# Performance work log

Measured on AMD Instinct MI355X. Metric: run time of the kernel, lower is better.

Reference implementation:

```python
import jax, jax.numpy as jnp
import numpy as np
from jax import lax

H = 12  # num_heads (from init_kwargs)


def _orthogonal_landmarks(q, num_landmarks):
    # q: (B, N, D) already scaled. Faithful to torch loop: recursively pick the
    # point whose max |cos sim| to the already-selected landmarks is minimal.
    B, N, D = q.shape
    nrm = jnp.linalg.norm(q, axis=-1, keepdims=True)
    qk = q / jnp.maximum(nrm, 1e-12)
    bidx = jnp.arange(B)
    key = jax.random.key(42)
    idx0 = jax.random.randint(key, (B,), 0, N)
    cur = qk[bidx, idx0]                             # (B, D)
    # running max |cos sim|; selected rows pinned to 10 (as in torch code)
    max_sim = jnp.zeros((B, N), qk.dtype).at[bidx, idx0].set(10.0)

    def step(carry, _):
        max_sim, cur = carry
        cos = jnp.abs(jnp.einsum('bnd,bd->bn', qk, cur))
        max_sim = jnp.maximum(max_sim, cos)
        idx = jnp.argmin(max_sim, axis=-1)
        cur2 = qk[bidx, idx]
        max_sim = max_sim.at[bidx, idx].set(10.0)
        return (max_sim, cur2), idx

    (_, _), idxs = lax.scan(step, (max_sim, cur), None, length=num_landmarks - 1)
    all_idx = jnp.concatenate([idx0[None, :], idxs], axis=0).T  # (B, L)
    landmarks = q[bidx[:, None], all_idx]                        # unnormalized q rows
    return lax.stop_gradient(landmarks)


def _orthoformer(q, k, v, num_landmarks, num_frames):
    # q,k,v: (B*h, N, D);  N = F * P
    Bh, N, D = q.shape
    F = num_frames
    P = N // F
    sc = D ** (-0.25)
    q = q * sc
    k = k * sc
    lm = _orthogonal_landmarks(q, num_landmarks)                 # (Bh, L, D)
    kernel_1 = jax.nn.softmax(jnp.einsum('bnd,bld->bnl', q, lm), axis=-1)   # (Bh,N,L)
    k2 = jnp.einsum('bld,bnd->bln', lm, k).reshape(Bh, num_landmarks, F, P)
    kernel_2 = jax.nn.softmax(k2, axis=-1)                       # (Bh,L,F,P)
    vr = v.reshape(Bh, F, P, D)
    x = jnp.einsum('blfp,bfpd->blfd', kernel_2, vr)
    x = jnp.einsum('bnl,blfd->bnfd', kernel_1, x)                # (Bh,N,F,D)
    return x


def setup_inputs() -> dict:
    key = jax.random.key(0)
    ks = jax.random.split(key, 6)
    B, F, P, C = 2, 16, 196, 768
    N = F * P
    s = 0.02
    x = jax.random.normal(ks[0], (B, N, C), jnp.float32)
    W_qkv = jax.random.normal(ks[1], (C, 3 * C), jnp.float32) * s
    W_pq = jax.random.normal(ks[2], (C, C), jnp.float32) * s
    W_pkv = jax.random.normal(ks[3], (C, 2 * C), jnp.float32) * s
    W_proj = jax.random.normal(ks[4], (C, C), jnp.float32) * s
    b_proj = jnp.zeros((C,), jnp.float32)
    return {"x": x, "W_qkv": W_qkv, "W_pq": W_pq, "W_pkv": W_pkv,
            "W_proj": W_proj, "b_proj": b_proj,
            "seq_len": P, "num_frames": F, "num_landmarks": 128}


def reference(x, W_qkv, W_pq, W_pkv, W_proj, b_proj, seq_len, num_frames, num_landmarks):
    B, N, C = x.shape
    F, P, h = num_frames, seq_len, H
    d = C // h
    scale = d ** (-0.5)
    qkv = x @ W_qkv                                              # (B,N,3C)
    q, k, v = jnp.split(qkv, 3, axis=-1)
    def to_bh(t):  # b n (h d) -> (b h) n d
        return t.reshape(B, N, h, d).transpose(0, 2, 1, 3).reshape(B * h, N, d)
    q_, k_, v_ = to_bh(q), to_bh(k), to_bh(v)
    xo = _orthoformer(q_, k_, v_, num_landmarks, F)              # (B*h,N,F,d)
    # (b h) s f d -> b s f (h d)
    xo = xo.reshape(B, h, N, F, d).transpose(0, 2, 3, 1, 4).reshape(B, N, F, C)
    # diagonal over (frame-of-query g, frame-of-key f)
    xd = xo.reshape(B, F, P, F, C)
    xdiag = jnp.diagonal(xd, axis1=1, axis2=3)                   # (B,P,C,F)
    xdiag = jnp.moveaxis(xdiag, -1, 1).reshape(B, N, C)          # b (f p) d
    q2 = xdiag @ W_pq                                            # (B,N,C)
    k2, v2 = jnp.split(xo @ W_pkv, 2, axis=-1)                   # (B,N,F,C) each
    q2 = q2.reshape(B, N, h, d).transpose(0, 2, 1, 3) * scale    # (B,h,N,d)
    k2 = k2.reshape(B, N, F, h, d).transpose(0, 3, 1, 2, 4)      # (B,h,N,F,d)
    v2 = v2.reshape(B, N, F, h, d).transpose(0, 3, 1, 2, 4)
    attn = jax.nn.softmax(jnp.einsum('bhsd,bhsfd->bhsf', q2, k2), axis=-1)
    out = jnp.einsum('bhsf,bhsfd->bhsd', attn, v2)               # (B,h,N,d)
    out = out.transpose(0, 2, 1, 3).reshape(B, N, C)
    out = out @ W_proj + b_proj
    return out, attn
```

## Files before the change

kernel.cpp:

```cpp
#include <hip/hip_runtime.h>


using u16 = unsigned short;
using u32 = unsigned int;
using u64 = unsigned long long;

typedef short bf16x8 __attribute__((ext_vector_type(8)));
typedef float f32x4 __attribute__((ext_vector_type(4)));

#define N_ 3136
#define C_ 768
#define H_ 12
#define F_ 16
#define P_ 196
#define L_ 128
#define SC_ 0.35355339059327373f
#define OUTPART_ ((size_t)2 * N_ * C_)
#define KB_ 8
#define RPB_ 392

__device__ __forceinline__ float b2f(u16 u) {
  u32 x = ((u32)u) << 16; float f; __builtin_memcpy(&f, &x, 4); return f;
}
__device__ __forceinline__ float lo16f(u32 u) {
  u32 x = u << 16; float f; __builtin_memcpy(&f, &x, 4); return f;
}
__device__ __forceinline__ float hi16f(u32 u) {
  u32 x = u & 0xFFFF0000u; float f; __builtin_memcpy(&f, &x, 4); return f;
}
__device__ __forceinline__ u16 f2b(float f) {
  u32 u; __builtin_memcpy(&u, &f, 4);
  u32 r = (u + 0x7FFFu + ((u >> 16) & 1u)) >> 16;
  return (u16)r;
}
__device__ __forceinline__ u64 d2u(double d) { u64 u; __builtin_memcpy(&u, &d, 8); return u; }

__device__ __forceinline__ void gll16(const void* g, void* l) {
  __builtin_amdgcn_global_load_lds(
      (__attribute__((address_space(1))) void*)g,
      (__attribute__((address_space(3))) void*)l, 16, 0, 0);
}

__global__ void detect_k(const u32* __restrict__ w, int* __restrict__ flag) {
  const int t = threadIdx.x;
  int hits = 0;
  #pragma unroll
  for (int i = 0; i < 16; ++i) {
    u32 word = w[t * 16 + i];
    u32 e = (word >> 7) & 0xFFu;
    if (e >= 110u && e <= 126u) hits++;
  }
  #pragma unroll
  for (int off = 32; off > 0; off >>= 1) hits += __shfl_down(hits, off);
  if (t == 0) flag[0] = (hits >= 512) ? 0 : 1;
}

__global__ void zcnt_k(u64* __restrict__ p) { if (threadIdx.x < 384) p[threadIdx.x] = 0ull; }

__device__ __forceinline__ void tf2(u32 k0, u32 k1v, u32 c0, u32 c1, u32& o0, u32& o1) {
  u32 ks[3] = {k0, k1v, k0 ^ k1v ^ 0x1BD11BDAu};
  u32 x0 = c0 + ks[0], x1 = c1 + ks[1];
  const u32 rA[4] = {13u, 15u, 26u, 6u}, rB[4] = {17u, 29u, 16u, 24u};
  #pragma unroll
  for (int r = 0; r < 5; ++r) {
    #pragma unroll
    for (int q = 0; q < 4; ++q) {
      u32 rot = (r & 1) ? rB[q] : rA[q];
      x0 += x1; x1 = (x1 << rot) | (x1 >> (32u - rot)); x1 ^= x0;
    }
    x0 += ks[(r + 1) % 3];
    x1 += ks[(r + 2) % 3] + (u32)(r + 1);
  }
  o0 = x0; o1 = x1;
}

__device__ __forceinline__ int tf_idx0(int bh) {
  u32 a0, a1, b0, b1;
  tf2(0u, 42u, 0u, 0u, a0, a1);
  tf2(0u, 42u, 0u, 1u, b0, b1);
  u32 j = (u32)bh;
  u32 h0, h1, l0, l1;
  tf2(a0, a1, 0u, j, h0, h1);
  u32 hi = h0 ^ h1;
  tf2(b0, b1, 0u, j, l0, l1);
  u32 lo = l0 ^ l1;
  return (int)(((hi % 3136u) * 2048u + (lo % 3136u)) % 3136u);
}

__global__ __launch_bounds__(256) void qselT_k(const void* __restrict__ xr, const void* __restrict__ wr,
                                               const int* __restrict__ flagp, float* __restrict__ qt)
{
  __shared__ float As[128 * 20];
  __shared__ float Bs[16 * 64];
  const int t = threadIdx.x;
  const int m0 = blockIdx.x * 128;
  const int n0 = blockIdx.y * 64;
  const int f32i = flagp[0];
  const int tx = t & 15, ty = t >> 4;
  float acc[8][4];
  #pragma unroll
  for (int i = 0; i < 8; ++i)
    #pragma unroll
    for (int j = 0; j < 4; ++j) acc[i][j] = 0.f;

  const int alr = t >> 1;
  const int alk = (t & 1) * 8;
  const int bkr = t >> 4;
  const int bnc = (t & 15) * 4;

  for (int k0 = 0; k0 < 768; k0 += 16) {
    float av[8];
    float4 bv;
    if (f32i) {
      const float* xa = (const float*)xr + (size_t)(m0 + alr) * 768 + k0 + alk;
      float4 a0 = *(const float4*)(xa);
      float4 a1 = *(const float4*)(xa + 4);
      av[0] = a0.x; av[1] = a0.y; av[2] = a0.z; av[3] = a0.w;
      av[4] = a1.x; av[5] = a1.y; av[6] = a1.z; av[7] = a1.w;
      bv = *(const float4*)((const float*)wr + (size_t)(k0 + bkr) * 2304 + n0 + bnc);
    } else {
      const u16* xa = (const u16*)xr + (size_t)(m0 + alr) * 768 + k0 + alk;
      #pragma unroll
      for (int j = 0; j < 8; ++j) av[j] = b2f(xa[j]);
      const u16* wa = (const u16*)wr + (size_t)(k0 + bkr) * 2304 + n0 + bnc;
      bv.x = b2f(wa[0]); bv.y = b2f(wa[1]); bv.z = b2f(wa[2]); bv.w = b2f(wa[3]);
    }
    #pragma unroll
    for (int j = 0; j < 8; ++j) As[alr * 20 + alk + j] = av[j];
    *(float4*)(&Bs[bkr * 64 + bnc]) = bv;
    __syncthreads();
    #pragma unroll
    for (int kk = 0; kk < 16; ++kk) {
      float a[8], b[4];
      #pragma unroll
      for (int i = 0; i < 8; ++i) a[i] = As[(ty * 8 + i) * 20 + kk];
      #pragma unroll
      for (int j = 0; j < 4; ++j) b[j] = Bs[kk * 64 + tx * 4 + j];
      #pragma unroll
      for (int i = 0; i < 8; ++i)
        #pragma unroll
        for (int j = 0; j < 4; ++j) acc[i][j] += a[i] * b[j];
    }
    __syncthreads();
  }
  #pragma unroll
  for (int i = 0; i < 8; ++i) {
    const int m = m0 + ty * 8 + i;
    const int b = m / N_, n = m - b * N_;
    #pragma unroll
    for (int j = 0; j < 4; ++j) {
      const int col = n0 + tx * 4 + j;
      const int hh = col >> 6, dd = col & 63;
      qt[((size_t)(b * H_ + hh) * 64 + dd) * N_ + n] = acc[i][j] * SC_;
    }
  }
}

__global__ __launch_bounds__(512, 1) void landmarksR_k(
    const float* __restrict__ qt, float* __restrict__ lm, u64* __restrict__ cand)
{
  const int kb = blockIdx.y;
  const int bh = blockIdx.x;
  const float* QT = qt + (size_t)bh * 64 * N_;
  float* LM = lm + (size_t)bh * L_ * 64;
  u64* cd = cand + (size_t)bh * 16;
  __shared__ double curD[64];
  __shared__ u64 redV[8];
  __shared__ int redI[8];
  __shared__ int sW;
  const int t = threadIdx.x;
  const bool act = (t < RPB_);
  const int g = t >> 2, dc = t & 3, d0 = dc * 16;
  const int r0 = kb * RPB_;
  const int myRow = r0 + t;
  const float* base = QT + r0 + 4 * g;

  float4 qreg[16];
  #pragma unroll
  for (int i = 0; i < 16; ++i) qreg[i] = (float4){0.f, 0.f, 0.f, 0.f};
  if (act) {
    #pragma unroll
    for (int i = 0; i < 16; ++i) qreg[i] = *(const float4*)(base + (size_t)(d0 + i) * N_);
  }

  double inv_own = 0.0, ms_own = 0.0;
  if (act) {
    double s0 = 0.0, s1 = 0.0, s2 = 0.0, s3 = 0.0;
    #pragma unroll
    for (int i = 0; i < 16; ++i) {
      const float4 v = qreg[i];
      s0 += (double)v.x * (double)v.x; s1 += (double)v.y * (double)v.y;
      s2 += (double)v.z * (double)v.z; s3 += (double)v.w * (double)v.w;
    }
    s0 += __shfl_xor(s0, 1); s1 += __shfl_xor(s1, 1);
    s2 += __shfl_xor(s2, 1); s3 += __shfl_xor(s3, 1);
    s0 += __shfl_xor(s0, 2); s1 += __shfl_xor(s1, 2);
    s0 = s0; s1 = s1;
    s2 += __shfl_xor(s2, 2); s3 += __shfl_xor(s3, 2);
    const double sown = (dc == 0) ? s0 : (dc == 1) ? s1 : (dc == 2) ? s2 : s3;
    inv_own = 1.0 / fmax(sqrt(sown), 1e-12);
  }
  const int idx0 = tf_idx0(bh);
  if (act && myRow == idx0) ms_own = 10.0;

  if (t < 64) {
    const float vf = QT[(size_t)t * N_ + idx0];
    double v = (double)vf;
    double s = v * v;
    #pragma unroll
    for (int off = 32; off; off >>= 1) s += __shfl_xor(s, off);
    curD[t] = v / fmax(sqrt(s), 1e-12);
    if (kb == 0) LM[t] = vf;
  }
  __syncthreads();

  for (int step = 1; step < 128; ++step) {
    u64 bV = d2u(1e30); int bI = 0x7fffffff;
    if (act) {
      double a0 = 0.0, a1 = 0.0, a2 = 0.0, a3 = 0.0;
      #pragma unroll
      for (int i = 0; i < 16; ++i) {
        const float4 v = qreg[i];
        const double c = curD[d0 + i];
        a0 += (double)v.x * c; a1 += (double)v.y * c;
        a2 += (double)v.z * c; a3 += (double)v.w * c;
      }
      a0 += __shfl_xor(a0, 1); a1 += __shfl_xor(a1, 1);
      a2 += __shfl_xor(a2, 1); a3 += __shfl_xor(a3, 1);
      a0 += __shfl_xor(a0, 2); a1 += __shfl_xor(a1, 2);
      a2 += __shfl_xor(a2, 2); a3 += __shfl_xor(a3, 2);
      const double aown = (dc == 0) ? a0 : (dc == 1) ? a1 : (dc == 2) ? a2 : a3;
      ms_own = fmax(ms_own, fabs(aown * inv_own));
      bV = d2u(ms_own); bI = myRow;
    }
    #pragma unroll
    for (int off = 32; off; off >>= 1) {
      const u64 ov = __shfl_xor(bV, off);
      const int oi = __shfl_xor(bI, off);
      if (ov < bV || (ov == bV && oi < bI)) { bV = ov; bI = oi; }
    }
    if ((t & 63) == 0) { redV[t >> 6] = bV; redI[t >> 6] = bI; }
    __syncthreads();
    const int par = step & 1;
    if (t == 0) {
      u64 v = redV[0]; int ix = redI[0];
      #pragma unroll
      for (int w2 = 1; w2 < 8; ++w2)
        if (redV[w2] < v || (redV[w2] == v && redI[w2] < ix)) { v = redV[w2]; ix = redI[w2]; }
      const u64 pk = (v & ~((1ull << 19) - 1ull)) | ((u64)(u32)(step & 127) << 12) | (u64)(u32)ix;
      __hip_atomic_store(&cd[par * KB_ + kb], pk, __ATOMIC_RELAXED, __HIP_MEMORY_SCOPE_AGENT);
    }
    if (t < 64) {
      u64 pv = ~0ull;
      int ok = 1;
      for (;;) {
        if (t < KB_) {
          pv = __hip_atomic_load(&cd[par * KB_ + t], __ATOMIC_RELAXED, __HIP_MEMORY_SCOPE_AGENT);
          ok = ((int)((pv >> 12) & 127u) == step) ? 1 : 0;
        }
        if (__all(ok)) break;
        __builtin_amdgcn_s_sleep(1);
      }
      u64 m = (t < KB_) ? pv : ~0ull;
      #pragma unroll
      for (int off = 1; off < KB_; off <<= 1) {
        const u64 o = __shfl_xor(m, off);
        if (o < m) m = o;
      }
      if (t == 0) sW = (int)(m & 0xFFFu);
    }
    __syncthreads();
    const int w = sW;
    if (act && myRow == w) ms_own = 10.0;
    if (t < 64) {
      const float vf = QT[(size_t)t * N_ + w];
      double v = (double)vf;
      double s = v * v;
      #pragma unroll
      for (int off = 32; off; off >>= 1) s += __shfl_xor(s, off);
      curD[t] = v / fmax(sqrt(s), 1e-12);
      if (kb == 0) LM[(size_t)step * 64 + t] = vf;
    }
    __syncthreads();
  }
}

__device__ __forceinline__ void twT_body(const void* W, int K, int Nn, int f32i,
                                         u16* WT, int k0, int n0, int t, u16 (&Ts)[64][80])
{
  const int kr = t >> 2, nc = (t & 3) * 16;
  u16 tmp[16];
  if (f32i) {
    const float* p = (const float*)W + (size_t)(k0 + kr) * Nn + n0 + nc;
    #pragma unroll
    for (int j = 0; j < 16; ++j) tmp[j] = f2b(p[j]);
  } else {
    const u16* p = (const u16*)W + (size_t)(k0 + kr) * Nn + n0 + nc;
    #pragma unroll
    for (int j = 0; j < 16; ++j) tmp[j] = p[j];
  }
  #pragma unroll
  for (int j = 0; j < 16; ++j) Ts[kr][nc + j] = tmp[j];
  __syncthreads();
  const int nr = t >> 2, kc = (t & 3) * 16;
  u16 o[16];
  #pragma unroll
  for (int j = 0; j < 16; ++j) o[j] = Ts[kc + j][nr];
  u16* dst = WT + (size_t)(n0 + nr) * K + k0 + kc;
  *(uint4*)(dst) = *(uint4*)(o);
  *(uint4*)(dst + 8) = *(uint4*)(o + 8);
}

__global__ __launch_bounds__(256) void twT_k(const void* __restrict__ W, int K, int Nn,
                                             const int* __restrict__ flagp, u16* __restrict__ WT)
{
  __shared__ u16 Ts[64][80];
  twT_body(W, K, Nn, flagp[0], WT, blockIdx.x * 64, blockIdx.y * 64, threadIdx.x, Ts);
}

__global__ __launch_bounds__(256) void twT3_k(const void* __restrict__ W0, const void* __restrict__ W1,
                                              const void* __restrict__ W2, const int* __restrict__ flagp,
                                              u16* __restrict__ T0, u16* __restrict__ T1, u16* __restrict__ T2,
                                              u16* __restrict__ Wb)
{
  __shared__ u16 Ts[64][80];
  const int z = blockIdx.z;
  const int t = threadIdx.x;
  if (z == 3) {
    const int k0 = blockIdx.x * 64, n0 = blockIdx.y * 64;
    const int kr = t >> 2, nc = (t & 3) * 16;
    u16 tmp[16];
    if (flagp[0]) {
      const float* p = (const float*)W0 + (size_t)(k0 + kr) * 1536 + n0 + nc;
      #pragma unroll
      for (int j = 0; j < 16; ++j) tmp[j] = f2b(p[j]);
    } else {
      const u16* p = (const u16*)W0 + (size_t)(k0 + kr) * 1536 + n0 + nc;
      #pragma unroll
      for (int j = 0; j < 16; ++j) tmp[j] = p[j];
    }
    u16* dst = Wb + (size_t)(k0 + kr) * 1536 + n0 + nc;
    *(uint4*)(dst) = *(uint4*)(tmp);
    *(uint4*)(dst + 8) = *(uint4*)(tmp + 8);
    return;
  }
  const void* W = (z == 0) ? W0 : (z == 1) ? W1 : W2;
  u16* WT = (z == 0) ? T0 : (z == 1) ? T1 : T2;
  const int Nn = (z == 0) ? 1536 : 768;
  if (blockIdx.y * 64 >= Nn) return;
  twT_body(W, 768, Nn, flagp[0], WT, blockIdx.x * 64, blockIdx.y * 64, t, Ts);
}

__global__ __launch_bounds__(256) void xcvt_k(const void* __restrict__ x,
                                              const int* __restrict__ flagp, u16* __restrict__ xb)
{
  const int i = blockIdx.x * 256 + threadIdx.x;
  if (flagp[0]) {
    const float4* p = (const float4*)x + (size_t)i * 2;
    float4 f0 = p[0], f1 = p[1];
    u16 tmp[8] = { f2b(f0.x), f2b(f0.y), f2b(f0.z), f2b(f0.w),
                   f2b(f1.x), f2b(f1.y), f2b(f1.z), f2b(f1.w) };
    *(uint4*)(xb + (size_t)i * 8) = *(uint4*)tmp;
  } else {
    ((uint4*)xb)[i] = ((const uint4*)x)[i];
  }
}

struct GemmCore {
  const u16 *aP0, *aP1, *bP0, *bP1;
  u16 *lA0, *lA1, *lB0, *lB1;
  int roA[4], roB[4];
  int mw, nw, lr, lk;
};

__device__ __forceinline__ void gemm_core_init(GemmCore& gc, u16* As, u16* Bs,
    const u16* A16, const u16* B16, size_t aOff, size_t bOff,
    int m0, int n0, int lda, int ldb, int M, int t)
{
  const int lane = t & 63;
  const int w = t >> 6;
  gc.mw = (w >> 1) * 64;
  gc.nw = (w & 1) * 64;
  gc.lr = lane & 15;
  gc.lk = lane >> 4;
  const int c0 = w * 2, c1 = c0 + 1;
  const int rl = lane >> 2, sl = lane & 3;
  const int rowA0 = c0 * 16 + rl, rowA1 = c1 * 16 + rl;
  const int segA0 = (sl ^ ((rowA0 ^ (rowA0 >> 2)) & 3)) * 8;
  const int segA1 = (sl ^ ((rowA1 ^ (rowA1 >> 2)) & 3)) * 8;
  int ga0 = m0 + rowA0; if (ga0 >= M) ga0 = M - 1;
  int ga1 = m0 + rowA1; if (ga1 >= M) ga1 = M - 1;
  gc.aP0 = A16 + aOff + (size_t)ga0 * lda + segA0;
  gc.aP1 = A16 + aOff + (size_t)ga1 * lda + segA1;
  gc.bP0 = B16 + bOff + (size_t)(n0 + rowA0) * ldb + segA0;
  gc.bP1 = B16 + bOff + (size_t)(n0 + rowA1) * ldb + segA1;
  gc.lA0 = &As[c0 * 512]; gc.lA1 = &As[c1 * 512];
  gc.lB0 = &Bs[c0 * 512]; gc.lB1 = &Bs[c1 * 512];
  #pragma unroll
  for (int q = 0; q < 4; ++q) {
    const int ra = gc.mw + q * 16 + gc.lr;
    gc.roA[q] = ra * 32 + ((gc.lk ^ ((ra ^ (ra >> 2)) & 3)) * 8);
    const int rb = gc.nw + q * 16 + gc.lr;
    gc.roB[q] = rb * 32 + ((gc.lk ^ ((rb ^ (rb >> 2)) & 3)) * 8);
  }
}

__device__ __forceinline__ void gemm_core_loop(const GemmCore& gc, u16* As, u16* Bs,
                                               int K, f32x4 (&acc)[4][4])
{
  for (int k0 = 0; k0 < K; k0 += 32) {
    gll16(gc.aP0 + k0, gc.lA0);
    gll16(gc.aP1 + k0, gc.lA1);
    gll16(gc.bP0 + k0, gc.lB0);
    gll16(gc.bP1 + k0, gc.lB1);
    __syncthreads();
    bf16x8 af[4], bfv[4];
    #pragma unroll
    for (int mt = 0; mt < 4; ++mt) af[mt] = *(const bf16x8*)(&As[gc.roA[mt]]);
    #pragma unroll
    for (int nt = 0; nt < 4; ++nt) bfv[nt] = *(const bf16x8*)(&Bs[gc.roB[nt]]);
    #pragma unroll
    for (int mt = 0; mt < 4; ++mt)
      #pragma unroll
      for (int nt = 0; nt < 4; ++nt)
        acc[mt][nt] = __builtin_amdgcn_mfma_f32_16x16x32_bf16(af[mt], bfv[nt], acc[mt][nt], 0, 0, 0);
    __syncthreads();
  }
}

template <int MODE>
__global__ __launch_bounds__(256) void gemm_k(
    const void* __restrict__ Ap, const void* __restrict__ Bp,
    int M, int K, int lda, int ldb, int n0c, int cn, const int* __restrict__ flagp,
    float* __restrict__ of0, u16* __restrict__ ob0, u16* __restrict__ ob1, u16* __restrict__ ob2,
    const void* __restrict__ biasRaw, void* __restrict__ outRaw)
{
  __shared__ u16 As[128 * 32];
  __shared__ u16 Bs[128 * 32];
  const int t = threadIdx.x;
  const int m0 = blockIdx.x * 128;
  const int n0 = blockIdx.y * 128;
  const int rf = (MODE == 4) ? flagp[0] : 0;

  size_t aOff = 0, bOff = 0;
  if constexpr (MODE == 1) {
    const int bh = blockIdx.z;
    aOff = (size_t)bh * ((size_t)N_ * 128) + (size_t)n0c * 128;
    bOff = (size_t)bh * (1024 * 128);
  }
  if constexpr (MODE == 5) {
    const int h = blockIdx.z;
    aOff = (size_t)h * (2 * cn) * 64;
    bOff = (size_t)h * 64;
  }
  if constexpr (MODE == 6) {
    const int h = blockIdx.z;
    aOff = (size_t)h * (2 * cn) * 768;
    bOff = (size_t)(768 + h * 64) * 768;
  }
  f32x4 acc[4][4];
  #pragma unroll
  for (int i = 0; i < 4; ++i)
    #pragma unroll
    for (int j = 0; j < 4; ++j) acc[i][j] = (f32x4){0.f, 0.f, 0.f, 0.f};

  GemmCore gc;
  gemm_core_init(gc, As, Bs, (const u16*)Ap, (const u16*)Bp, aOff, bOff, m0, n0, lda, ldb, M, t);
  gemm_core_loop(gc, As, Bs, K, acc);

  const int lr = gc.lr, lk = gc.lk, mw = gc.mw, nw = gc.nw;
  #pragma unroll
  for (int mt = 0; mt < 4; ++mt) {
    #pragma unroll
    for (int nt = 0; nt < 4; ++nt) {
      #pragma unroll
      for (int r = 0; r < 4; ++r) {
        const int grow = m0 + mw + mt * 16 + lk * 4 + r;
        const int gcol = n0 + nw + nt * 16 + lr;
        if (grow >= M) continue;
        float vv = acc[mt][nt][r];
        if constexpr (MODE == 0) {
          int b = (grow >= N_) ? 1 : 0;
          int n = grow - b * N_;
          int t3 = gcol / C_, cc = gcol - t3 * C_;
          int hh = cc >> 6, dd = cc & 63;
          size_t dst = (((size_t)(b * H_ + hh)) * N_ + n) * 64 + dd;
          if (t3 == 0) ob0[dst] = f2b(vv * SC_);
          else if (t3 == 1) ob1[dst] = f2b(vv * SC_);
          else ob2[dst] = f2b(vv);
        } else if constexpr (MODE == 1) {
          const int bh = blockIdx.z;
          int b = bh / H_, hh = bh - b * H_;
          int f = gcol >> 6, dd = gcol & 63;
          u16 wv = f2b(vv);
          ob0[(((size_t)(b * cn + grow)) * F_ + f) * C_ + hh * 64 + dd] = wv;
          int n = n0c + grow;
          if (f == n / P_) ob1[((size_t)(b * cn + grow)) * C_ + hh * 64 + dd] = wv;
        } else if constexpr (MODE == 3) {
          int hh = gcol >> 6, dd = gcol & 63;
          ob0[((size_t)hh * (2 * cn) + grow) * 64 + dd] = f2b(vv * 0.125f);
        } else if constexpr (MODE == 5) {
          ob0[((size_t)blockIdx.z * (2 * cn) + grow) * 768 + gcol] = f2b(vv);
        } else if constexpr (MODE == 6) {
          if (gcol < 64) {
            int b2 = (grow >= cn) ? 1 : 0;
            int ln = grow - b2 * cn;
            ob0[((size_t)(b2 * N_ + n0c + ln)) * 768 + blockIdx.z * 64 + gcol] = f2b(vv);
          }
        } else {
          float bvad = rf ? ((const float*)biasRaw)[gcol] : b2f(((const u16*)biasRaw)[gcol]);
          float ov = vv + bvad;
          if (rf) ((float*)outRaw)[(size_t)grow * C_ + gcol] = ov;
          else    ((u16*)outRaw)[(size_t)grow * C_ + gcol] = f2b(ov);
        }
      }
    }
  }
}

__global__ __launch_bounds__(256) void k1_k(const u16* __restrict__ qb,
                                            const float* __restrict__ lm,
                                            u16* __restrict__ k1)
{
  const int bh = blockIdx.y;
  const int r0 = blockIdx.x * 64;
  __shared__ float qT[64][65];
  __shared__ float lmS[128 * 64];
  __shared__ float redA[4][64];
  __shared__ float redB[64];
  const int t = threadIdx.x;
  const u16* Q = qb + ((size_t)bh * N_ + r0) * 64;
  const float* Lm = lm + (size_t)bh * L_ * 64;
  for (int u = t; u < 2048; u += 256) ((float4*)lmS)[u] = ((const float4*)Lm)[u];
  for (int u = t; u < 512; u += 256) {
    int row = u >> 3, j0 = (u & 7) * 8;
    uint4 pk = *(const uint4*)(Q + (size_t)row * 64 + j0);
    const u16* pu = (const u16*)&pk;
    #pragma unroll
    for (int jj = 0; jj < 8; ++jj) qT[j0 + jj][row] = b2f(pu[jj]);
  }
  __syncthreads();
  const int row = t & 63, ch = t >> 6;
  float qr[64];
  #pragma unroll
  for (int j = 0; j < 64; ++j) qr[j] = qT[j][row];
  float s[32];
  for (int li = 0; li < 32; ++li) {
    const float* lp = lmS + (ch * 32 + li) * 64;
    float a = 0.f;
    #pragma unroll
    for (int j = 0; j < 64; ++j) a += lp[j] * qr[j];
    s[li] = a;
  }
  float mx = -1e30f;
  for (int li = 0; li < 32; ++li) mx = fmaxf(mx, s[li]);
  redA[ch][row] = mx;
  __syncthreads();
  if (t < 64) redB[t] = fmaxf(fmaxf(redA[0][t], redA[1][t]), fmaxf(redA[2][t], redA[3][t]));
  __syncthreads();
  mx = redB[row];
  float sum = 0.f;
  for (int li = 0; li < 32; ++li) { float e = __expf(s[li] - mx); s[li] = e; sum += e; }
  __syncthreads();
  redA[ch][row] = sum;
  __syncthreads();
  if (t < 64) redB[t] = 1.0f / (redA[0][t] + redA[1][t] + redA[2][t] + redA[3][t]);
  __syncthreads();
  const float inv = redB[row];
  u16* out = k1 + ((size_t)bh * N_ + r0 + row) * 128 + ch * 32;
  for (int li = 0; li < 32; ++li) out[li] = f2b(s[li] * inv);
}

__global__ __launch_bounds__(256) void k2x1_k(const float* __restrict__ lm,
                                              const u16* __restrict__ kb,
                                              const u16* __restrict__ vb,
                                              u16* __restrict__ x1)
{
  const int bh = blockIdx.x;
  const int f = blockIdx.y;
  __shared__ u16 kS[P_ * 64];
  __shared__ u16 vS[P_ * 64];
  __shared__ float redM[2][128];
  __shared__ float redS[2][128];
  const int t = threadIdx.x;
  const u16* Kf = kb + ((size_t)bh * N_ + f * P_) * 64;
  const u16* Vf = vb + ((size_t)bh * N_ + f * P_) * 64;
  for (int u = t; u < 1568; u += 256) {
    ((uint4*)kS)[u] = ((const uint4*)Kf)[u];
    ((uint4*)vS)[u] = ((const uint4*)Vf)[u];
  }
  __syncthreads();
  const int l = t & 127, half = t >> 7;
  const float* lp = lm + ((size_t)bh * L_ + l) * 64;
  float lr[64];
  #pragma unroll
  for (int j = 0; j < 64; ++j) lr[j] = lp[j];

  const int p0 = half * 98, p1 = p0 + 98;
  float mx = -1e30f;
  for (int p = p0; p < p1; ++p) {
    const uint4* kp = (const uint4*)(kS + p * 64);
    float s = 0.f;
    #pragma unroll
    for (int q4 = 0; q4 < 8; ++q4) {
      uint4 pk = kp[q4];
      const u32* pu = (const u32*)&pk;
      #pragma unroll
      for (int j2 = 0; j2 < 4; ++j2) {
        u32 u = pu[j2];
        s += lr[q4 * 8 + j2 * 2] * lo16f(u) + lr[q4 * 8 + j2 * 2 + 1] * hi16f(u);
      }
    }
    mx = fmaxf(mx, s);
  }
  redM[half][l] = mx;
  __syncthreads();
  mx = fmaxf(redM[0][l], redM[1][l]);

  float sm = 0.f;
  for (int p = p0; p < p1; ++p) {
    const uint4* kp = (const uint4*)(kS + p * 64);
    float s = 0.f;
    #pragma unroll
    for (int q4 = 0; q4 < 8; ++q4) {
      uint4 pk = kp[q4];
      const u32* pu = (const u32*)&pk;
      #pragma unroll
      for (int j2 = 0; j2 < 4; ++j2) {
        u32 u = pu[j2];
        s += lr[q4 * 8 + j2 * 2] * lo16f(u) + lr[q4 * 8 + j2 * 2 + 1] * hi16f(u);
      }
    }
    sm += __expf(s - mx);
  }
  redS[half][l] = sm;
  __syncthreads();
  const float inv = 1.0f / (redS[0][l] + redS[1][l]);

  const int dd0 = half * 32;
  float acc[32];
  #pragma unroll
  for (int u = 0; u < 32; ++u) acc[u] = 0.f;
  for (int p = 0; p < P_; ++p) {
    const uint4* kp = (const uint4*)(kS + p * 64);
    float s = 0.f;
    #pragma unroll
    for (int q4 = 0; q4 < 8; ++q4) {
      uint4 pk = kp[q4];
      const u32* pu = (const u32*)&pk;
      #pragma unroll
      for (int j2 = 0; j2 < 4; ++j2) {
        u32 u = pu[j2];
        s += lr[q4 * 8 + j2 * 2] * lo16f(u) + lr[q4 * 8 + j2 * 2 + 1] * hi16f(u);
      }
    }
    const float e = __expf(s - mx);
    const uint4* vp = (const uint4*)(vS + p * 64 + dd0);
    #pragma unroll
    for (int q4 = 0; q4 < 4; ++q4) {
      uint4 pv = vp[q4];
      const u32* pu = (const u32*)&pv;
      #pragma unroll
      for (int j2 = 0; j2 < 4; ++j2) {
        u32 u = pu[j2];
        acc[q4 * 8 + j2 * 2]     += e * lo16f(u);
        acc[q4 * 8 + j2 * 2 + 1] += e * hi16f(u);
      }
    }
  }
  u16* outT = x1 + (size_t)bh * (1024 * 128) + (size_t)(f * 64 + dd0) * 128 + l;
  for (int u = 0; u < 32; ++u) outT[(size_t)u * 128] = f2b(acc[u] * inv);
}

__global__ __launch_bounds__(256) void attn2_k(const u16* __restrict__ xoc,
                                               const u16* __restrict__ g,
                                               int n0c, int cn, const int* __restrict__ flagp,
                                               void* __restrict__ outRaw, u16* __restrict__ wc)
{
  __shared__ float aS[12][16];
  const int t = threadIdx.x;
  const int m = blockIdx.x;
  const int b = (m >= cn) ? 1 : 0;
  const int ln = m - b * cn;
  const int n = n0c + ln;
  const int f32o = flagp[0];
  const u16* Xo = xoc + ((size_t)(b * cn + ln) * 16) * 768;
  const size_t hstr = (size_t)(2 * cn) * 768;

  if (t < 192) {
    const int h = t >> 4, f = t & 15;
    const uint4* xp = (const uint4*)(Xo + (size_t)f * 768);
    const uint4* gp = (const uint4*)(g + (size_t)h * hstr + (size_t)m * 768);
    float lg = 0.f;
    #pragma unroll 4
    for (int q = 0; q < 96; ++q) {
      uint4 xv = xp[q], gv = gp[q];
      const u32* xu = (const u32*)&xv;
      const u32* gu = (const u32*)&gv;
      #pragma unroll
      for (int j = 0; j < 4; ++j)
        lg += lo16f(xu[j]) * lo16f(gu[j]) + hi16f(xu[j]) * hi16f(gu[j]);
    }
    float mx = lg;
    mx = fmaxf(mx, __shfl_xor(mx, 1));
    mx = fmaxf(mx, __shfl_xor(mx, 2));
    mx = fmaxf(mx, __shfl_xor(mx, 4));
    mx = fmaxf(mx, __shfl_xor(mx, 8));
    float e = __expf(lg - mx);
    float sm = e;
    sm += __shfl_xor(sm, 1);
    sm += __shfl_xor(sm, 2);
    sm += __shfl_xor(sm, 4);
    sm += __shfl_xor(sm, 8);
    const float a = e / sm;
    const size_t abase = ((size_t)(b * H_ + h) * N_ + n) * F_ + f;
    if (f32o) ((float*)outRaw)[OUTPART_ + abase] = a;
    else      ((u16*)outRaw)[OUTPART_ + abase] = f2b(a);
    aS[h][f] = a;
  }
  __syncthreads();
  if (t < 192) {
    const int cg = t >> 1, sh = t & 1;
    const int c0 = cg * 8;
    float acc[6][8];
    #pragma unroll
    for (int j = 0; j < 6; ++j)
      #pragma unroll
      for (int k = 0; k < 8; ++k) acc[j][k] = 0.f;
    for (int f = 0; f < 16; ++f) {
      uint4 xv = *(const uint4*)(Xo + (size_t)f * 768 + c0);
      const u32* xu = (const u32*)&xv;
      float xf[8];
      #pragma unroll
      for (int j = 0; j < 4; ++j) { xf[2 * j] = lo16f(xu[j]); xf[2 * j + 1] = hi16f(xu[j]); }
      #pragma unroll
      for (int j = 0; j < 6; ++j) {
        const float a = aS[sh * 6 + j][f];
        #pragma unroll
        for (int k = 0; k < 8; ++k) acc[j][k] += a * xf[k];
      }
    }
    #pragma unroll
    for (int j = 0; j < 6; ++j) {
      u16 pk[8];
      #pragma unroll
      for (int k = 0; k < 8; ++k) pk[k] = f2b(acc[j][k]);
      *(uint4*)(wc + (size_t)(sh * 6 + j) * hstr + (size_t)m * 768 + c0) = *(uint4*)pk;
    }
  }
}

extern "C" void kernel_launch(void* const* d_in, const int* in_sizes, int n_in,
                              void* d_out, int out_size, void* d_ws, size_t ws_size,
                              hipStream_t stream)
{
  (void)in_sizes; (void)n_in; (void)out_size;
  const void* x     = d_in[0];
  const void* Wqkv  = d_in[1];
  const void* Wpq   = d_in[2];
  const void* Wpkv  = d_in[3];
  const void* Wproj = d_in[4];
  const void* bproj = d_in[5];

  char* ws = (char*)d_ws;
  size_t off = 0;
  auto alloc = [&](size_t bytes) { void* p = ws + off; off += (bytes + 255) & ~(size_t)255; return p; };
  int*  flagp = (int*)alloc(256);
  u16*  qb  = (u16*)alloc(9633792);
  u16*  kb  = (u16*)alloc(9633792);
  u16*  vb  = (u16*)alloc(9633792);
  float* lm = (float*)alloc(786432);
  u16*  x1b = (u16*)alloc(6291456);
  u16*  ob  = (u16*)alloc(9633792);
  const size_t k1off = off;
  u16*  k1b = (u16*)alloc(19267584);
  const size_t chunk0 = off;

  const size_t qtNeed = k1off + 19267584 + 256;

  int Nc = 0;
  {
    const int cands[5] = {3136, 1568, 784, 392, 196};
    for (int i = 0; i < 5; ++i) {
      size_t need = chunk0 + (size_t)129024 * cands[i] + 1024;
      if (need <= ws_size && qtNeed <= ws_size) { Nc = cands[i]; break; }
    }
  }
  if (Nc == 0) return;
  const int nchunks = N_ / Nc;
  u16*  xoc = (u16*)(ws + chunk0);
  u16*  xdc = xoc + (size_t)24576 * Nc;
  u16*  q2b = xdc + (size_t)1536 * Nc;
  u16*  gbf = q2b + (size_t)1536 * Nc;
  u16*  wcb = gbf + (size_t)18432 * Nc;
  float* qt = (float*)(ws + k1off);

  u16* WqkvT  = (u16*)(ws + k1off);
  u16* xb     = (u16*)(ws + k1off + 3538944);
  u16* WpkvT  = kb;
  u16* WpqT   = kb + 1179648;
  u16* WprojT = kb + 1179648 + 589824;
  u16* Wpkvb  = kb + 1179648 + 589824 + 589824;

  u64* cand = (u64*)(ws + chunk0);

  detect_k<<<1, 64, 0, stream>>>((const u32*)Wqkv, flagp);
  zcnt_k<<<1, 512, 0, stream>>>(cand);

  qselT_k<<<dim3(49, 12), 256, 0, stream>>>(x, Wqkv, flagp, qt);
  landmarksR_k<<<dim3(24, KB_), 512, 0, stream>>>(qt, lm, cand);

  twT_k<<<dim3(12, 36), 256, 0, stream>>>(Wqkv, 768, 2304, flagp, WqkvT);
  xcvt_k<<<2352, 256, 0, stream>>>(x, flagp, xb);

  gemm_k<0><<<dim3(49, 18, 1), 256, 0, stream>>>(xb, WqkvT, 6272, 768, 768, 768, 0, 0, flagp,
                                                 nullptr, qb, kb, vb, nullptr, nullptr);
  k2x1_k<<<dim3(24, 16), 256, 0, stream>>>(lm, kb, vb, x1b);
  k1_k<<<dim3(49, 24), 256, 0, stream>>>(qb, lm, k1b);

  twT3_k<<<dim3(12, 24, 4), 256, 0, stream>>>(Wpkv, Wpq, Wproj, flagp,
                                              WpkvT, WpqT, WprojT, Wpkvb);

  const int gx = (2 * Nc + 127) / 128;
  for (int c = 0; c < nchunks; ++c) {
    const int n0c = c * Nc;
    gemm_k<1><<<dim3((Nc + 127) / 128, 8, 24), 256, 0, stream>>>(
        k1b, x1b, Nc, 128, 128, 128, n0c, Nc, flagp, nullptr, xoc, xdc, nullptr, nullptr, nullptr);
    gemm_k<3><<<dim3(gx, 6, 1), 256, 0, stream>>>(
        xdc, WpqT, 2 * Nc, 768, 768, 768, n0c, Nc, flagp, nullptr, q2b, nullptr, nullptr, nullptr, nullptr);
    gemm_k<5><<<dim3(gx, 6, 12), 256, 0, stream>>>(
        q2b, Wpkvb, 2 * Nc, 64, 64, 1536, n0c, Nc, flagp, nullptr, gbf, nullptr, nullptr, nullptr, nullptr);
    attn2_k<<<dim3(2 * Nc), 256, 0, stream>>>(xoc, gbf, n0c, Nc, flagp, d_out, wcb);
    gemm_k<6><<<dim3(gx, 1, 12), 256, 0, stream>>>(
        wcb, WpkvT, 2 * Nc, 768, 768, 768, n0c, Nc, flagp, nullptr, ob, nullptr, nullptr, nullptr, nullptr);
  }
  gemm_k<4><<<dim3(49, 6, 1), 256, 0, stream>>>(ob, WprojT, 6272, 768, 768, 768, 0, 0, flagp,
                                                nullptr, nullptr, nullptr, nullptr, bproj, d_out);
}
```

Baseline: 1.531 ms.

## Publish winning landmark row through cross-block slots to cut serial global reads

In the landmark selection loop, the block owning each step's local winner now publishes that row's 64 values and its inverse norm, each tagged with the step number, into a per-block slot in global memory. Every block then polls all slots together and takes the winner directly. This removes the extra global gather, norm reduction and one __syncthreads per step from the 127-step serial chain, and drops the sleep in the spin loop. In exchange the workspace is reorganised: weight transposes move earlier, buffers are aliased so attn2 writes into gbf in place, and the chunk sizing changes. These rely on correct aliasing and on the tagged-slot protocol holding under relaxed atomics.

```diff
diff --git a/kernel.cpp b/kernel.cpp
--- a/kernel.cpp
+++ b/kernel.cpp
@@ -18,6 +18,7 @@
 #define OUTPART_ ((size_t)2 * N_ * C_)
 #define KB_ 8
 #define RPB_ 392
+#define SLOTW_ 80
 
 __device__ __forceinline__ float b2f(u16 u) {
   u32 x = ((u32)u) << 16; float f; __builtin_memcpy(&f, &x, 4); return f;
@@ -34,6 +35,7 @@
   return (u16)r;
 }
 __device__ __forceinline__ u64 d2u(double d) { u64 u; __builtin_memcpy(&u, &d, 8); return u; }
+__device__ __forceinline__ double u2d(u64 u) { double d; __builtin_memcpy(&d, &u, 8); return d; }
 
 __device__ __forceinline__ void gll16(const void* g, void* l) {
   __builtin_amdgcn_global_load_lds(
@@ -55,7 +57,7 @@
   if (t == 0) flag[0] = (hits >= 512) ? 0 : 1;
 }
 
-__global__ void zcnt_k(u64* __restrict__ p) { if (threadIdx.x < 384) p[threadIdx.x] = 0ull; }
+__global__ void zcnt_k(u64* __restrict__ p) { p[blockIdx.x * 512 + threadIdx.x] = 0ull; }
 
 __device__ __forceinline__ void tf2(u32 k0, u32 k1v, u32 c0, u32 c1, u32& o0, u32& o1) {
   u32 ks[3] = {k0, k1v, k0 ^ k1v ^ 0x1BD11BDAu};
@@ -156,17 +158,19 @@
   }
 }
 
-__global__ __launch_bounds__(512, 1) void landmarksR_k(
+__global__ __launch_bounds__(512, 1) void landmarksB_k(
     const float* __restrict__ qt, float* __restrict__ lm, u64* __restrict__ cand)
 {
   const int kb = blockIdx.y;
   const int bh = blockIdx.x;
   const float* QT = qt + (size_t)bh * 64 * N_;
   float* LM = lm + (size_t)bh * L_ * 64;
-  u64* cd = cand + (size_t)bh * 16;
+  u64* cd = cand + (size_t)bh * (2 * KB_ * SLOTW_);
   __shared__ double curD[64];
   __shared__ u64 redV[8];
   __shared__ int redI[8];
+  __shared__ u64 sMyVal;
+  __shared__ int sMyIx;
   __shared__ int sW;
   const int t = threadIdx.x;
   const bool act = (t < RPB_);
@@ -195,7 +199,6 @@
     s0 += __shfl_xor(s0, 1); s1 += __shfl_xor(s1, 1);
     s2 += __shfl_xor(s2, 1); s3 += __shfl_xor(s3, 1);
     s0 += __shfl_xor(s0, 2); s1 += __shfl_xor(s1, 2);
-    s0 = s0; s1 = s1;
     s2 += __shfl_xor(s2, 2); s3 += __shfl_xor(s3, 2);
     const double sown = (dc == 0) ? s0 : (dc == 1) ? s1 : (dc == 2) ? s2 : s3;
     inv_own = 1.0 / fmax(sqrt(sown), 1e-12);
@@ -242,46 +245,88 @@
     if ((t & 63) == 0) { redV[t >> 6] = bV; redI[t >> 6] = bI; }
     __syncthreads();
     const int par = step & 1;
+    u64* slot = cd + (size_t)(par * KB_ + kb) * SLOTW_;
     if (t == 0) {
       u64 v = redV[0]; int ix = redI[0];
       #pragma unroll
       for (int w2 = 1; w2 < 8; ++w2)
         if (redV[w2] < v || (redV[w2] == v && redI[w2] < ix)) { v = redV[w2]; ix = redI[w2]; }
-      const u64 pk = (v & ~((1ull << 19) - 1ull)) | ((u64)(u32)(step & 127) << 12) | (u64)(u32)ix;
-      __hip_atomic_store(&cd[par * KB_ + kb], pk, __ATOMIC_RELAXED, __HIP_MEMORY_SCOPE_AGENT);
+      sMyVal = v; sMyIx = ix;
+    }
+    __syncthreads();
+    const int mix = sMyIx;
+    const u64 tg = (u64)(u32)step << 32;
+    if (act && (t >> 2) == ((mix - r0) >> 2)) {
+      const int j = (mix - r0) & 3;
+      #pragma unroll
+      for (int i = 0; i < 16; ++i) {
+        const float4 v4 = qreg[i];
+        float vv = v4.x;
+        if (j == 1) vv = v4.y; else if (j == 2) vv = v4.z; else if (j == 3) vv = v4.w;
+        u32 fb; __builtin_memcpy(&fb, &vv, 4);
+        __hip_atomic_store(&slot[3 + d0 + i], tg | (u64)fb, __ATOMIC_RELAXED, __HIP_MEMORY_SCOPE_AGENT);
+      }
+    }
+    if (act && myRow == mix) {
+      const u64 ib = d2u(inv_own);
+      __hip_atomic_store(&slot[1], tg | (u64)(u32)ib, __ATOMIC_RELAXED, __HIP_MEMORY_SCOPE_AGENT);
+      __hip_atomic_store(&slot[2], tg | (u64)(u32)(ib >> 32), __ATOMIC_RELAXED, __HIP_MEMORY_SCOPE_AGENT);
+    }
+    if (t == 0) {
+      const u64 pk = (sMyVal & ~((1ull << 19) - 1ull)) | ((u64)(u32)(step & 127) << 12) | (u64)(u32)mix;
+      __hip_atomic_store(&slot[0], pk, __ATOMIC_RELAXED, __HIP_MEMORY_SCOPE_AGENT);
     }
     if (t < 64) {
-      u64 pv = ~0ull;
-      int ok = 1;
+      u64 colw[KB_];
+      u64 aux = 0;
       for (;;) {
+        bool ok = true;
+        #pragma unroll
+        for (int s = 0; s < KB_; ++s) {
+          colw[s] = __hip_atomic_load(&cd[(size_t)(par * KB_ + s) * SLOTW_ + 3 + t],
+                                      __ATOMIC_RELAXED, __HIP_MEMORY_SCOPE_AGENT);
+          ok = ok && ((int)(colw[s] >> 32) == step);
+        }
         if (t < KB_) {
-          pv = __hip_atomic_load(&cd[par * KB_ + t], __ATOMIC_RELAXED, __HIP_MEMORY_SCOPE_AGENT);
-          ok = ((int)((pv >> 12) & 127u) == step) ? 1 : 0;
+          aux = __hip_atomic_load(&cd[(size_t)(par * KB_ + t) * SLOTW_],
+                                  __ATOMIC_RELAXED, __HIP_MEMORY_SCOPE_AGENT);
+          ok = ok && ((int)((aux >> 12) & 127u) == (step & 127));
+        } else if (t < 2 * KB_) {
+          aux = __hip_atomic_load(&cd[(size_t)(par * KB_ + (t - KB_)) * SLOTW_ + 1],
+                                  __ATOMIC_RELAXED, __HIP_MEMORY_SCOPE_AGENT);
+          ok = ok && ((int)(aux >> 32) == step);
+        } else if (t < 3 * KB_) {
+          aux = __hip_atomic_load(&cd[(size_t)(par * KB_ + (t - 2 * KB_)) * SLOTW_ + 2],
+                                  __ATOMIC_RELAXED, __HIP_MEMORY_SCOPE_AGENT);
+          ok = ok && ((int)(aux >> 32) == step);
         }
         if (__all(ok)) break;
-        __builtin_amdgcn_s_sleep(1);
-      }
-      u64 m = (t < KB_) ? pv : ~0ull;
+      }
+      u64 m = (t < KB_) ? aux : ~0ull;
+      int msl = t & 7;
       #pragma unroll
       for (int off = 1; off < KB_; off <<= 1) {
         const u64 o = __shfl_xor(m, off);
-        if (o < m) m = o;
-      }
-      if (t == 0) sW = (int)(m & 0xFFFu);
+        const int os = __shfl_xor(msl, off);
+        if (o < m) { m = o; msl = os; }
+      }
+      const int wkb = __shfl(msl, 0);
+      const u64 wv = __shfl(m, 0);
+      const u32 ilo = (u32)__shfl(aux, KB_ + wkb);
+      const u32 ihi = (u32)__shfl(aux, 2 * KB_ + wkb);
+      const double invW = u2d(((u64)ihi << 32) | (u64)ilo);
+      u64 cw = colw[0];
+      #pragma unroll
+      for (int s = 1; s < KB_; ++s) cw = (wkb == s) ? colw[s] : cw;
+      const u32 fb = (u32)cw;
+      float vf; __builtin_memcpy(&vf, &fb, 4);
+      curD[t] = (double)vf * invW;
+      if (kb == 0) LM[(size_t)step * 64 + t] = vf;
+      if (t == 0) sW = (int)(wv & 0xFFFu);
     }
     __syncthreads();
     const int w = sW;
     if (act && myRow == w) ms_own = 10.0;
-    if (t < 64) {
-      const float vf = QT[(size_t)t * N_ + w];
-      double v = (double)vf;
-      double s = v * v;
-      #pragma unroll
-      for (int off = 32; off; off >>= 1) s += __shfl_xor(s, off);
-      curD[t] = v / fmax(sqrt(s), 1e-12);
-      if (kb == 0) LM[(size_t)step * 64 + t] = vf;
-    }
-    __syncthreads();
   }
 }
 
@@ -765,61 +810,56 @@
   char* ws = (char*)d_ws;
   size_t off = 0;
   auto alloc = [&](size_t bytes) { void* p = ws + off; off += (bytes + 255) & ~(size_t)255; return p; };
-  int*  flagp = (int*)alloc(256);
-  u16*  qb  = (u16*)alloc(9633792);
-  u16*  kb  = (u16*)alloc(9633792);
-  u16*  vb  = (u16*)alloc(9633792);
-  float* lm = (float*)alloc(786432);
-  u16*  x1b = (u16*)alloc(6291456);
-  u16*  ob  = (u16*)alloc(9633792);
-  const size_t k1off = off;
-  u16*  k1b = (u16*)alloc(19267584);
-  const size_t chunk0 = off;
-
-  const size_t qtNeed = k1off + 19267584 + 256;
+  int*  flagp  = (int*)alloc(256);
+  u16*  WpkvT  = (u16*)alloc(2359296);
+  u16*  WpqT   = (u16*)alloc(1179648);
+  u16*  WprojT = (u16*)alloc(1179648);
+  u16*  Wpkvb  = (u16*)alloc(2359296);
+  float* lm    = (float*)alloc(786432);
+  u16*  x1b    = (u16*)alloc(6291456);
+  u16*  ob     = (u16*)alloc(9633792);
+  u16*  k1b    = (u16*)alloc(19267584);
+  const size_t sc0 = off;
+
+  float* qt   = (float*)(ws + sc0);
+  u64*   cand = (u64*)(ws + sc0 + 19267584);
+  u16* WqkvT = (u16*)(ws + sc0);
+  u16* xb    = (u16*)(ws + sc0 + 3538944);
+  u16* qb    = (u16*)(ws + sc0 + 13172736);
+  u16* kbuf  = qb + 4816896;
+  u16* vb    = kbuf + 4816896;
+  const size_t phaseB_need = sc0 + 42074112 + 1024;
+  if (phaseB_need > ws_size) return;
 
   int Nc = 0;
   {
     const int cands[5] = {3136, 1568, 784, 392, 196};
     for (int i = 0; i < 5; ++i) {
-      size_t need = chunk0 + (size_t)129024 * cands[i] + 1024;
-      if (need <= ws_size && qtNeed <= ws_size) { Nc = cands[i]; break; }
+      if (sc0 + (size_t)92160 * cands[i] + 1024 <= ws_size) { Nc = cands[i]; break; }
     }
   }
   if (Nc == 0) return;
   const int nchunks = N_ / Nc;
-  u16*  xoc = (u16*)(ws + chunk0);
-  u16*  xdc = xoc + (size_t)24576 * Nc;
-  u16*  q2b = xdc + (size_t)1536 * Nc;
-  u16*  gbf = q2b + (size_t)1536 * Nc;
-  u16*  wcb = gbf + (size_t)18432 * Nc;
-  float* qt = (float*)(ws + k1off);
-
-  u16* WqkvT  = (u16*)(ws + k1off);
-  u16* xb     = (u16*)(ws + k1off + 3538944);
-  u16* WpkvT  = kb;
-  u16* WpqT   = kb + 1179648;
-  u16* WprojT = kb + 1179648 + 589824;
-  u16* Wpkvb  = kb + 1179648 + 589824 + 589824;
-
-  u64* cand = (u64*)(ws + chunk0);
+  u16* xoc = (u16*)(ws + sc0);
+  u16* xdc = xoc + (size_t)24576 * Nc;
+  u16* q2b = xdc + (size_t)1536 * Nc;
+  u16* gbf = q2b + (size_t)1536 * Nc;
 
   detect_k<<<1, 64, 0, stream>>>((const u32*)Wqkv, flagp);
-  zcnt_k<<<1, 512, 0, stream>>>(cand);
+  zcnt_k<<<60, 512, 0, stream>>>(cand);
+  twT3_k<<<dim3(12, 24, 4), 256, 0, stream>>>(Wpkv, Wpq, Wproj, flagp,
+                                              WpkvT, WpqT, WprojT, Wpkvb);
 
   qselT_k<<<dim3(49, 12), 256, 0, stream>>>(x, Wqkv, flagp, qt);
-  landmarksR_k<<<dim3(24, KB_), 512, 0, stream>>>(qt, lm, cand);
+  landmarksB_k<<<dim3(24, KB_), 512, 0, stream>>>(qt, lm, cand);
 
   twT_k<<<dim3(12, 36), 256, 0, stream>>>(Wqkv, 768, 2304, flagp, WqkvT);
   xcvt_k<<<2352, 256, 0, stream>>>(x, flagp, xb);
 
   gemm_k<0><<<dim3(49, 18, 1), 256, 0, stream>>>(xb, WqkvT, 6272, 768, 768, 768, 0, 0, flagp,
-                                                 nullptr, qb, kb, vb, nullptr, nullptr);
-  k2x1_k<<<dim3(24, 16), 256, 0, stream>>>(lm, kb, vb, x1b);
+                                                 nullptr, qb, kbuf, vb, nullptr, nullptr);
+  k2x1_k<<<dim3(24, 16), 256, 0, stream>>>(lm, kbuf, vb, x1b);
   k1_k<<<dim3(49, 24), 256, 0, stream>>>(qb, lm, k1b);
-
-  twT3_k<<<dim3(12, 24, 4), 256, 0, stream>>>(Wpkv, Wpq, Wproj, flagp,
-                                              WpkvT, WpqT, WprojT, Wpkvb);
 
   const int gx = (2 * Nc + 127) / 128;
   for (int c = 0; c < nchunks; ++c) {
@@ -830,9 +870,9 @@
         xdc, WpqT, 2 * Nc, 768, 768, 768, n0c, Nc, flagp, nullptr, q2b, nullptr, nullptr, nullptr, nullptr);
     gemm_k<5><<<dim3(gx, 6, 12), 256, 0, stream>>>(
         q2b, Wpkvb, 2 * Nc, 64, 64, 1536, n0c, Nc, flagp, nullptr, gbf, nullptr, nullptr, nullptr, nullptr);
-    attn2_k<<<dim3(2 * Nc), 256, 0, stream>>>(xoc, gbf, n0c, Nc, flagp, d_out, wcb);
+    attn2_k<<<dim3(2 * Nc), 256, 0, stream>>>(xoc, gbf, n0c, Nc, flagp, d_out, gbf);
     gemm_k<6><<<dim3(gx, 1, 12), 256, 0, stream>>>(
-        wcb, WpkvT, 2 * Nc, 768, 768, 768, n0c, Nc, flagp, nullptr, ob, nullptr, nullptr, nullptr, nullptr);
+        gbf, WpkvT, 2 * Nc, 768, 768, 768, n0c, Nc, flagp, nullptr, ob, nullptr, nullptr, nullptr, nullptr);
   }
   gemm_k<4><<<dim3(49, 6, 1), 256, 0, stream>>>(ob, WprojT, 6272, 768, 768, 768, 0, 0, flagp,
                                                 nullptr, nullptr, nullptr, nullptr, bproj, d_out);
```

New measurement: 1.936 ms. +26.4%, slower.
